# Kernel optimization log

Hardware: AMD Instinct MI355X
Metric: run time of the kernel (lower is better)

Reference implementation:

```python
import jax, jax.numpy as jnp
import numpy as np

N = 20000
E = 600000
D = 512
H = 8
HD = D // H
HID = 1024
FIN = D + 3 * H  # forces_mlp input dim = 536
SCALE = 1.0 / float(np.sqrt(HD))


def _ln(x, g, b, eps=1e-5):
    m = x.mean(-1, keepdims=True)
    v = x.var(-1, keepdims=True)
    return (x - m) / jnp.sqrt(v + eps) * g + b


def _resmlp(h, Wi, bi, Wh, bh, Wo, bo):
    # ResMLP with layers=3: in-proj, one residual hidden block, out-proj
    h = jax.nn.gelu(h @ Wi + bi)
    h = h + jax.nn.gelu(h @ Wh + bh)
    return h @ Wo + bo


def setup_inputs() -> dict:
    key = jax.random.key(0)
    ks = jax.random.split(key, 24)
    s = 0.02
    x = jax.random.normal(ks[0], (N, D), jnp.float32)
    edge_index = jax.random.randint(ks[1], (2, E), 0, N, dtype=jnp.int32)
    att_bias = jax.random.normal(ks[2], (E,), jnp.float32)
    pos = jax.random.normal(ks[3], (N, 3), jnp.float32)
    batch = jnp.zeros((N,), jnp.int32)
    return {
        "x": x, "edge_index": edge_index, "att_bias": att_bias, "pos": pos, "batch": batch,
        "g_att": jnp.ones((D,), jnp.float32), "b_att": jnp.zeros((D,), jnp.float32),
        "g_mlp": jnp.ones((D,), jnp.float32), "b_mlp": jnp.zeros((D,), jnp.float32),
        "Wq": jax.random.normal(ks[4], (D, D), jnp.float32) * s, "bq": jnp.zeros((D,), jnp.float32),
        "Wk": jax.random.normal(ks[5], (D, D), jnp.float32) * s, "bk": jnp.zeros((D,), jnp.float32),
        "We_in": jax.random.normal(ks[6], (D, HID), jnp.float32) * s, "be_in": jnp.zeros((HID,), jnp.float32),
        "We_h": jax.random.normal(ks[7], (HID, HID), jnp.float32) * s, "be_h": jnp.zeros((HID,), jnp.float32),
        "We_out": jax.random.normal(ks[8], (HID, 1), jnp.float32) * s, "be_out": jnp.zeros((1,), jnp.float32),
        "Wf_in": jax.random.normal(ks[9], (FIN, HID), jnp.float32) * s, "bf_in": jnp.zeros((HID,), jnp.float32),
        "Wf_h": jax.random.normal(ks[10], (HID, HID), jnp.float32) * s, "bf_h": jnp.zeros((HID,), jnp.float32),
        "Wf_out": jax.random.normal(ks[11], (HID, 3), jnp.float32) * s, "bf_out": jnp.zeros((3,), jnp.float32),
    }


def reference(x, edge_index, att_bias, pos, batch,
              g_att, b_att, g_mlp, b_mlp, Wq, bq, Wk, bk,
              We_in, be_in, We_h, be_h, We_out, be_out,
              Wf_in, bf_in, Wf_h, bf_h, Wf_out, bf_out):
    n = x.shape[0]
    row, col = edge_index[0], edge_index[1]

    z_att = _ln(x, g_att, b_att)
    q = (z_att @ Wq + bq).reshape(n, H, HD)  # [N,H,HD]
    k = (z_att @ Wk + bk).reshape(n, H, HD)

    # sparse scaled dot product restricted to edges, with additive per-edge bias
    logits = jnp.einsum('ehd,ehd->eh', q[row], k[col]) * SCALE + att_bias[:, None]  # [E,H]
    mx = jax.ops.segment_max(logits, row, num_segments=n)          # [N,H]
    mx = jnp.where(jnp.isfinite(mx), mx, 0.0)
    p = jnp.exp(logits - mx[row])
    denom = jax.ops.segment_sum(p, row, num_segments=n)            # [N,H]
    w = p / denom[row]                                             # [E,H]

    contrib = jnp.einsum('eh,ec->ehc', w, pos[col])                # [E,H,3]
    att = jax.ops.segment_sum(contrib, row, num_segments=n)        # [N,H,3]
    att = att - pos[:, None, :]                                    # att - value
    att = att.reshape(n, H * 3)                                    # permute(1,0,2).view(N,-1)

    z_mlp = _ln(x, g_mlp, b_mlp)
    energy = _resmlp(z_mlp, We_in, be_in, We_h, be_h, We_out, be_out)
    forces = _resmlp(jnp.concatenate([z_mlp, att], axis=-1), Wf_in, bf_in, Wf_h, bf_h, Wf_out, bf_out)
    return (energy, forces)
```

## Files before the change

### kernel.cpp

```cpp
#include <hip/hip_runtime.h>

#define NN 20000
#define EE 600000

typedef unsigned short u16;
typedef unsigned int u32;
typedef float f32x4 __attribute__((ext_vector_type(4)));
typedef u32 u32x4 __attribute__((ext_vector_type(4)));

__device__ __forceinline__ u16 f2bf(float f){
  u32 u = __float_as_uint(f);
  return (u16)((u + 0x7fffu + ((u>>16)&1u))>>16);
}
__device__ __forceinline__ float bf2f(u16 h){ return __uint_as_float(((u32)h)<<16); }

__device__ __forceinline__ float gelu_f(float x){
  float u = 0.7978845608028654f*(x + 0.044715f*x*x*x);
  float e = __expf(2.0f*u);
  return 0.5f*x*(2.0f - 2.0f/(e+1.0f));
}

__global__ __launch_bounds__(256) void ln2_kernel(
    const float* __restrict__ x,
    const float* __restrict__ ga, const float* __restrict__ ba,
    const float* __restrict__ gm, const float* __restrict__ bm,
    u16* __restrict__ za, u16* __restrict__ xf, int N)
{
  int row = (blockIdx.x<<2) + (threadIdx.x>>6);
  int lane = threadIdx.x & 63;
  if(row >= N) return;
  const float* xp = x + ((size_t)row<<9) + (lane<<3);
  f32x4 v0 = *(const f32x4*)xp;
  f32x4 v1 = *(const f32x4*)(xp+4);
  float vals[8] = {v0[0],v0[1],v0[2],v0[3],v1[0],v1[1],v1[2],v1[3]};
  float s=0.f, qs=0.f;
#pragma unroll
  for(int i=0;i<8;i++){ s += vals[i]; qs = fmaf(vals[i],vals[i],qs); }
#pragma unroll
  for(int o=1;o<64;o<<=1){ s += __shfl_xor(s,o); qs += __shfl_xor(qs,o); }
  float mean = s*(1.f/512.f);
  float var  = qs*(1.f/512.f) - mean*mean;
  float rstd = rsqrtf(var + 1e-5f);
  int c0 = lane<<3;
#pragma unroll
  for(int i=0;i<8;i++){
    float zn = (vals[i]-mean)*rstd;
    za[((size_t)row<<9)+c0+i]  = f2bf(fmaf(zn, ga[c0+i], ba[c0+i]));
    xf[(size_t)row*576+c0+i]   = f2bf(fmaf(zn, gm[c0+i], bm[c0+i]));
  }
}

__global__ __launch_bounds__(256) void wtt_kernel(
    const float* __restrict__ W, u16* __restrict__ WT, int K, int Nn, int Kpad)
{
  __shared__ u16 tile[64][65];
  const int k0 = blockIdx.x<<6, n0 = blockIdx.y<<6;
  const int tx = threadIdx.x & 63, ty = threadIdx.x >> 6;
#pragma unroll
  for(int i=0;i<16;i++){
    int r = (i<<2) + ty;
    int gk = k0 + r;
    float v = (gk < K) ? W[(size_t)gk*Nn + n0 + tx] : 0.f;
    tile[r][tx] = f2bf(v);
  }
  __syncthreads();
#pragma unroll
  for(int i=0;i<16;i++){
    int r = (i<<2) + ty;
    WT[(size_t)(n0 + r)*Kpad + k0 + tx] = tile[tx][r];
  }
}

__global__ __launch_bounds__(256) void gemm_bt(
    const u16* __restrict__ A, const u16* __restrict__ B,
    const float* __restrict__ bias, const u16* __restrict__ resid,
    u16* __restrict__ Cb, const float* __restrict__ wout,
    float* __restrict__ outp,
    int M, int N, int K, int lda, int ldr, int mode)
{
  __shared__ u16 As[128*64];
  __shared__ u16 Bs[128*64];
  const int gx = gridDim.x;
  const int b  = blockIdx.y*gx + blockIdx.x;
  const int xcd = b & 7, loc = b >> 3;
  const int tileM = ((loc/gx)*8 + xcd) << 7;
  const int tileN = (loc % gx) << 7;
  if(tileM >= M) return;
  const int tid  = threadIdx.x;
  const int wave = tid>>6, lane = tid&63;
  const int quad = lane>>4, l15 = lane&15;
  const int mhalf = (wave>>1)<<6, nhalf = (wave&1)<<6;
  f32x4 acc[4][4] = {};

  for(int k0=0; k0<K; k0+=64){
#pragma unroll
    for(int j=0;j<4;j++){
      const int c   = (((wave<<2)+j)<<6) + lane;
      const int row = c>>3;
      const int cc  = (c&7) ^ (row&7);
      int gr = tileM + row; gr = (gr < M) ? gr : (M-1);
      const u16* gp = A + (size_t)gr*lda + (size_t)(k0 + (cc<<3));
      __builtin_amdgcn_global_load_lds(
        (const __attribute__((address_space(1))) u32*)gp,
        (__attribute__((address_space(3))) u32*)(&As[((wave<<2)+j)<<9]),
        16, 0, 0);
    }
#pragma unroll
    for(int j=0;j<4;j++){
      const int c   = (((wave<<2)+j)<<6) + lane;
      const int row = c>>3;
      const int cc  = (c&7) ^ (row&7);
      const u16* gp = B + (size_t)(tileN + row)*K + (size_t)(k0 + (cc<<3));
      __builtin_amdgcn_global_load_lds(
        (const __attribute__((address_space(1))) u32*)gp,
        (__attribute__((address_space(3))) u32*)(&Bs[((wave<<2)+j)<<9]),
        16, 0, 0);
    }
    __syncthreads();
#pragma unroll
    for(int ks=0;ks<2;ks++){
      const int ccol = (ks<<2) + quad;
      u32x4 af[4], bfr[4];
#pragma unroll
      for(int mi=0;mi<4;mi++){
        const int row = mhalf + (mi<<4) + l15;
        af[mi] = *(const u32x4*)&As[((row<<3) + (ccol ^ (row&7)))<<3];
      }
#pragma unroll
      for(int ni=0;ni<4;ni++){
        const int row = nhalf + (ni<<4) + l15;
        bfr[ni] = *(const u32x4*)&Bs[((row<<3) + (ccol ^ (row&7)))<<3];
      }
#pragma unroll
      for(int mi=0;mi<4;mi++)
#pragma unroll
        for(int ni=0;ni<4;ni++)
          asm("v_mfma_f32_16x16x32_bf16 %0, %1, %2, %0"
              : "+v"(acc[mi][ni]) : "v"(af[mi]), "v"(bfr[ni]));
    }
    __syncthreads();
  }

  if(mode <= 1){
#pragma unroll
    for(int mi=0;mi<4;mi++){
#pragma unroll
      for(int reg=0;reg<4;reg++){
        const int gr = tileM + mhalf + (mi<<4) + (quad<<2) + reg;
        if(gr < M){
#pragma unroll
          for(int ni=0;ni<4;ni++){
            const int gc = tileN + nhalf + (ni<<4) + l15;
            float v = acc[mi][ni][reg] + bias[gc];
            if(mode == 1) v = gelu_f(v);
            Cb[(size_t)gr*N + gc] = f2bf(v);
          }
        }
      }
    }
  } else if(mode == 2){
    float wv[4], bv[4];
#pragma unroll
    for(int ni=0;ni<4;ni++){
      int gc = tileN + nhalf + (ni<<4) + l15;
      wv[ni] = wout[gc]; bv[ni] = bias[gc];
    }
#pragma unroll
    for(int mi=0;mi<4;mi++){
#pragma unroll
      for(int reg=0;reg<4;reg++){
        const int gr = tileM + mhalf + (mi<<4) + (quad<<2) + reg;
        if(gr < M){
          float vs = 0.f;
#pragma unroll
          for(int ni=0;ni<4;ni++){
            const int gc = tileN + nhalf + (ni<<4) + l15;
            float v = gelu_f(acc[mi][ni][reg] + bv[ni])
                    + bf2f(resid[(size_t)gr*ldr + gc]);
            vs = fmaf(v, wv[ni], vs);
          }
          vs += __shfl_xor(vs,1); vs += __shfl_xor(vs,2);
          vs += __shfl_xor(vs,4); vs += __shfl_xor(vs,8);
          if(l15 == 0) atomicAdd(&outp[gr], vs);
        }
      }
    }
  } else {
    float wv0[4], wv1[4], wv2[4], bv[4];
#pragma unroll
    for(int ni=0;ni<4;ni++){
      int gc = tileN + nhalf + (ni<<4) + l15;
      wv0[ni] = wout[gc*3+0]; wv1[ni] = wout[gc*3+1]; wv2[ni] = wout[gc*3+2];
      bv[ni] = bias[gc];
    }
#pragma unroll
    for(int mi=0;mi<4;mi++){
#pragma unroll
      for(int reg=0;reg<4;reg++){
        const int gr = tileM + mhalf + (mi<<4) + (quad<<2) + reg;
        if(gr < M){
          float s0=0.f, s1=0.f, s2=0.f;
#pragma unroll
          for(int ni=0;ni<4;ni++){
            const int gc = tileN + nhalf + (ni<<4) + l15;
            float v = gelu_f(acc[mi][ni][reg] + bv[ni])
                    + bf2f(resid[(size_t)gr*ldr + gc]);
            s0 = fmaf(v, wv0[ni], s0);
            s1 = fmaf(v, wv1[ni], s1);
            s2 = fmaf(v, wv2[ni], s2);
          }
          s0 += __shfl_xor(s0,1); s0 += __shfl_xor(s0,2); s0 += __shfl_xor(s0,4); s0 += __shfl_xor(s0,8);
          s1 += __shfl_xor(s1,1); s1 += __shfl_xor(s1,2); s1 += __shfl_xor(s1,4); s1 += __shfl_xor(s1,8);
          s2 += __shfl_xor(s2,1); s2 += __shfl_xor(s2,2); s2 += __shfl_xor(s2,4); s2 += __shfl_xor(s2,8);
          if(l15 == 0){
            atomicAdd(&outp[(size_t)gr*3+0], s0);
            atomicAdd(&outp[(size_t)gr*3+1], s1);
            atomicAdd(&outp[(size_t)gr*3+2], s2);
          }
        }
      }
    }
  }
}

__global__ __launch_bounds__(256) void out_init_kernel(
    float* __restrict__ out, const float* __restrict__ beO,
    const float* __restrict__ bfO)
{
  int idx = blockIdx.x*256 + threadIdx.x;
  if(idx < NN) out[idx] = beO[0];
  else if(idx < NN*4) out[idx] = bfO[(idx - NN) % 3];
}

__global__ __launch_bounds__(256) void hist_kernel(
    const int* __restrict__ ei, int* __restrict__ deg, int E)
{
  int e = blockIdx.x*256 + threadIdx.x;
  if(e < E) atomicAdd(&deg[ei[e]], 1);
}

__global__ __launch_bounds__(1024) void scan_kernel(
    const int* __restrict__ deg, int* __restrict__ rowptr,
    int* __restrict__ cursor, int N)
{
  __shared__ int wsum[16];
  __shared__ int carry_s;
  const int tid = threadIdx.x, lane = tid & 63, wid = tid >> 6;
  if(tid == 0) carry_s = 0;
  __syncthreads();
  for(int base = 0; base < N; base += 1024){
    int idx = base + tid;
    int v = (idx < N) ? deg[idx] : 0;
    int s = v;
#pragma unroll
    for(int o=1;o<64;o<<=1){ int t = __shfl_up(s,o); if(lane>=o) s += t; }
    if(lane==63) wsum[wid] = s;
    __syncthreads();
    if(wid==0 && lane<16){
      int ws = wsum[lane];
      int t = ws;
#pragma unroll
      for(int o=1;o<16;o<<=1){ int u = __shfl_up(t,o); if(lane>=o) t += u; }
      wsum[lane] = t - ws;
    }
    __syncthreads();
    int ex = s - v + wsum[wid] + carry_s;
    if(idx < N){ rowptr[idx] = ex; cursor[idx] = ex; }
    __syncthreads();
    if(tid == 1023) carry_s += wsum[15] + s;
  }
  __syncthreads();
  if(tid == 0) rowptr[N] = carry_s;
}

__global__ __launch_bounds__(256) void scatter_kernel(
    const int* __restrict__ ei, const float* __restrict__ ab,
    int* __restrict__ cursor, int* __restrict__ cols,
    float* __restrict__ abs_, int E)
{
  int e = blockIdx.x*256 + threadIdx.x;
  if(e >= E) return;
  int r = ei[e];
  int p = atomicAdd(&cursor[r], 1);
  cols[p] = ei[EE + e];
  abs_[p] = ab[e];
}

__global__ __launch_bounds__(256) void node_att_kernel(
    const u16* __restrict__ qk, const int* __restrict__ rowptr,
    const int* __restrict__ cols, const float* __restrict__ abs_,
    const float* __restrict__ pos, u16* __restrict__ xf, int N)
{
  const int node = (blockIdx.x<<2) + (threadIdx.x>>6);
  const int lane = threadIdx.x & 63;
  if(node >= N) return;
  const int h = lane>>3, sub = lane&7;
  const u32x4 qv = *(const u32x4*)(qk + ((size_t)node<<10) + (lane<<3));
  const float posn = (sub<3) ? pos[node*3 + sub] : 0.f;
  const int j1 = rowptr[node+1];
  float den = 0.f, nm = 0.f;

  int j = rowptr[node];
  for(; j+3 < j1; j += 4){
    int c[4]; float abv[4], pv[4]; u32x4 kv[4];
#pragma unroll
    for(int t=0;t<4;t++){ c[t] = cols[j+t]; abv[t] = abs_[j+t]; }
#pragma unroll
    for(int t=0;t<4;t++){
      kv[t] = *(const u32x4*)(qk + ((size_t)c[t]<<10) + 512 + (lane<<3));
      pv[t] = (sub<3) ? pos[c[t]*3+sub] : 0.f;
    }
#pragma unroll
    for(int t=0;t<4;t++){
      float s = 0.f;
#pragma unroll
      for(int i=0;i<4;i++){
        s = fmaf(__uint_as_float(qv[i]<<16),         __uint_as_float(kv[t][i]<<16), s);
        s = fmaf(__uint_as_float(qv[i]&0xffff0000u), __uint_as_float(kv[t][i]&0xffff0000u), s);
      }
      s += __shfl_xor(s,1); s += __shfl_xor(s,2); s += __shfl_xor(s,4);
      float p = __expf(fmaf(s, 0.125f, abv[t]));
      den += p;
      nm = fmaf(p, pv[t], nm);
    }
  }
  for(; j < j1; j++){
    int c0 = cols[j];
    u32x4 kv0 = *(const u32x4*)(qk + ((size_t)c0<<10) + 512 + (lane<<3));
    float pv0 = (sub<3) ? pos[c0*3+sub] : 0.f;
    float s0=0.f;
#pragma unroll
    for(int i=0;i<4;i++){
      s0 = fmaf(__uint_as_float(qv[i]<<16),        __uint_as_float(kv0[i]<<16), s0);
      s0 = fmaf(__uint_as_float(qv[i]&0xffff0000u),__uint_as_float(kv0[i]&0xffff0000u), s0);
    }
    s0 += __shfl_xor(s0,1); s0 += __shfl_xor(s0,2); s0 += __shfl_xor(s0,4);
    float p0 = __expf(fmaf(s0, 0.125f, abs_[j]));
    den += p0;
    nm = fmaf(p0, pv0, nm);
  }

  u16* xp = xf + (size_t)node*576;
  if(sub < 3){
    float a = (den > 0.f) ? nm/den : 0.f;
    xp[512 + h*3 + sub] = f2bf(a - posn);
  } else {
    xp[536 + h*5 + (sub-3)] = 0;
  }
}

extern "C" void kernel_launch(void* const* d_in, const int* in_sizes, int n_in,
                              void* d_out, int out_size, void* d_ws, size_t ws_size,
                              hipStream_t stream)
{
  (void)in_sizes; (void)n_in; (void)out_size; (void)ws_size;
  const float* x    = (const float*)d_in[0];
  const int*   ei   = (const int*)d_in[1];
  const float* ab   = (const float*)d_in[2];
  const float* pos  = (const float*)d_in[3];
  const float* g_att= (const float*)d_in[5];
  const float* b_att= (const float*)d_in[6];
  const float* g_mlp= (const float*)d_in[7];
  const float* b_mlp= (const float*)d_in[8];
  const float* Wq   = (const float*)d_in[9];  const float* bq  = (const float*)d_in[10];
  const float* Wk   = (const float*)d_in[11]; const float* bk  = (const float*)d_in[12];
  const float* WeI  = (const float*)d_in[13]; const float* beI = (const float*)d_in[14];
  const float* WeH  = (const float*)d_in[15]; const float* beH = (const float*)d_in[16];
  const float* WeO  = (const float*)d_in[17]; const float* beO = (const float*)d_in[18];
  const float* WfI  = (const float*)d_in[19]; const float* bfI = (const float*)d_in[20];
  const float* WfH  = (const float*)d_in[21]; const float* bfH = (const float*)d_in[22];
  const float* WfO  = (const float*)d_in[23]; const float* bfO = (const float*)d_in[24];

  char* w = (char*)d_ws;
  size_t off = 0;
  auto alloc = [&](size_t bytes) -> void* {
    void* p = w + off; off += (bytes + 255) & ~(size_t)255; return p;
  };
  u16* zatt  = (u16*)alloc((size_t)NN*512*2);
  u16* qk    = (u16*)alloc((size_t)NN*1024*2);
  u16* xf    = (u16*)alloc((size_t)NN*576*2);
  u16* h1cat = (u16*)alloc((size_t)NN*2048*2);
  u16* wqkT  = (u16*)alloc((size_t)1024*512*2);
  u16* wInT  = (u16*)alloc((size_t)2048*576*2);
  u16* weHT  = (u16*)alloc((size_t)1024*1024*2);
  u16* wfHT  = (u16*)alloc((size_t)1024*1024*2);
  float* bqk    = (float*)alloc((size_t)1024*4);
  float* bcat   = (float*)alloc((size_t)2048*4);
  int*   deg    = (int*)alloc((size_t)NN*4);
  int*   rowptr = (int*)alloc((size_t)(NN+1)*4);
  int*   cursor = (int*)alloc((size_t)NN*4);
  int*   cols   = (int*)alloc((size_t)EE*4);
  float* absrt  = (float*)alloc((size_t)EE*4);

  hipMemsetAsync(deg, 0, (size_t)NN*4, stream);
  hipMemcpyAsync(bqk,        bq,  512*4, hipMemcpyDeviceToDevice, stream);
  hipMemcpyAsync(bqk + 512,  bk,  512*4, hipMemcpyDeviceToDevice, stream);
  hipMemcpyAsync(bcat,       beI, 1024*4, hipMemcpyDeviceToDevice, stream);
  hipMemcpyAsync(bcat + 1024,bfI, 1024*4, hipMemcpyDeviceToDevice, stream);

  wtt_kernel<<<dim3(512/64, 512/64),256,0,stream>>>(Wq, wqkT,           512, 512, 512);
  wtt_kernel<<<dim3(512/64, 512/64),256,0,stream>>>(Wk, wqkT + 512*512, 512, 512, 512);
  wtt_kernel<<<dim3(576/64, 1024/64),256,0,stream>>>(WeI, wInT,              512, 1024, 576);
  wtt_kernel<<<dim3(576/64, 1024/64),256,0,stream>>>(WfI, wInT + 1024*576,   536, 1024, 576);
  wtt_kernel<<<dim3(1024/64,1024/64),256,0,stream>>>(WeH, weHT, 1024, 1024, 1024);
  wtt_kernel<<<dim3(1024/64,1024/64),256,0,stream>>>(WfH, wfHT, 1024, 1024, 1024);

  out_init_kernel<<<dim3((NN*4+255)/256),256,0,stream>>>((float*)d_out, beO, bfO);

  ln2_kernel<<<dim3((NN+3)/4),256,0,stream>>>(x, g_att,b_att, g_mlp,b_mlp, zatt, xf, NN);

  hist_kernel   <<<dim3((EE+255)/256),256,0,stream>>>(ei, deg, EE);
  scan_kernel   <<<1,1024,0,stream>>>(deg, rowptr, cursor, NN);
  scatter_kernel<<<dim3((EE+255)/256),256,0,stream>>>(ei, ab, cursor, cols, absrt, EE);

  const int MT = 160;

  gemm_bt<<<dim3(8, MT),256,0,stream>>>(zatt, wqkT, bqk, nullptr, qk,
                                        nullptr, nullptr, NN, 1024, 512, 512, 0, 0);

  node_att_kernel<<<dim3((NN+3)/4),256,0,stream>>>(qk, rowptr, cols, absrt, pos, xf, NN);

  gemm_bt<<<dim3(16, MT),256,0,stream>>>(xf, wInT, bcat, nullptr, h1cat,
                                         nullptr, nullptr, NN, 2048, 576, 576, 0, 1);

  gemm_bt<<<dim3(8, MT),256,0,stream>>>(h1cat, weHT, beH, h1cat, nullptr,
                                        WeO, (float*)d_out,
                                        NN, 1024, 1024, 2048, 2048, 2);
  gemm_bt<<<dim3(8, MT),256,0,stream>>>(h1cat+1024, wfHT, bfH, h1cat+1024, nullptr,
                                        WfO, (float*)d_out + NN,
                                        NN, 1024, 1024, 2048, 2048, 3);
}
```

Before: 639.0 us.

## Batch weight transposes and setup copies into fewer launches; unroll edge loop by 8

The six weight-transpose launches are merged into one 3D-grid kernel that reads per-matrix descriptors, with out-of-range blocks exiting early. The memset, four bias memcpys and the output-init kernel are folded into a single prep kernel. The per-node attention edge loop is unrolled from 4 to 8 edges so more gathers are in flight. Together these cut launch and API overhead and raise memory-level parallelism, at the cost of more registers in the attention kernel.

```diff
diff --git a/kernel.cpp b/kernel.cpp
--- a/kernel.cpp
+++ b/kernel.cpp
@@ -50,25 +50,45 @@
   }
 }
 
-__global__ __launch_bounds__(256) void wtt_kernel(
-    const float* __restrict__ W, u16* __restrict__ WT, int K, int Nn, int Kpad)
+struct WttDesc { const float* W; u16* WT; int K, Nn, Kpad; };
+struct WttPack { WttDesc d[6]; };
+
+__global__ __launch_bounds__(256) void wtt_all_kernel(WttPack p)
 {
   __shared__ u16 tile[64][65];
+  const WttDesc dd = p.d[blockIdx.z];
   const int k0 = blockIdx.x<<6, n0 = blockIdx.y<<6;
+  if(k0 >= dd.Kpad || n0 >= dd.Nn) return;
   const int tx = threadIdx.x & 63, ty = threadIdx.x >> 6;
 #pragma unroll
   for(int i=0;i<16;i++){
     int r = (i<<2) + ty;
     int gk = k0 + r;
-    float v = (gk < K) ? W[(size_t)gk*Nn + n0 + tx] : 0.f;
+    float v = (gk < dd.K) ? dd.W[(size_t)gk*dd.Nn + n0 + tx] : 0.f;
     tile[r][tx] = f2bf(v);
   }
   __syncthreads();
 #pragma unroll
   for(int i=0;i<16;i++){
     int r = (i<<2) + ty;
-    WT[(size_t)(n0 + r)*Kpad + k0 + tx] = tile[tx][r];
-  }
+    dd.WT[(size_t)(n0 + r)*dd.Kpad + k0 + tx] = tile[tx][r];
+  }
+}
+
+__global__ __launch_bounds__(256) void prep_kernel(
+    float* __restrict__ out, const float* __restrict__ beO, const float* __restrict__ bfO,
+    float* __restrict__ bqk, const float* __restrict__ bq, const float* __restrict__ bk,
+    float* __restrict__ bcat, const float* __restrict__ beI, const float* __restrict__ bfI,
+    int* __restrict__ deg)
+{
+  int idx = blockIdx.x*256 + threadIdx.x;
+  if(idx < NN) out[idx] = beO[0];
+  else if(idx < NN*4) out[idx] = bfO[(idx - NN) % 3];
+  if(idx < 512) bqk[idx] = bq[idx];
+  else if(idx < 1024) bqk[idx] = bk[idx-512];
+  if(idx < 1024) bcat[idx] = beI[idx];
+  else if(idx < 2048) bcat[idx] = bfI[idx-1024];
+  if(idx < NN) deg[idx] = 0;
 }
 
 __global__ __launch_bounds__(256) void gemm_bt(
@@ -223,15 +243,6 @@
   }
 }
 
-__global__ __launch_bounds__(256) void out_init_kernel(
-    float* __restrict__ out, const float* __restrict__ beO,
-    const float* __restrict__ bfO)
-{
-  int idx = blockIdx.x*256 + threadIdx.x;
-  if(idx < NN) out[idx] = beO[0];
-  else if(idx < NN*4) out[idx] = bfO[(idx - NN) % 3];
-}
-
 __global__ __launch_bounds__(256) void hist_kernel(
     const int* __restrict__ ei, int* __restrict__ deg, int E)
 {
@@ -301,17 +312,17 @@
   float den = 0.f, nm = 0.f;
 
   int j = rowptr[node];
-  for(; j+3 < j1; j += 4){
-    int c[4]; float abv[4], pv[4]; u32x4 kv[4];
-#pragma unroll
-    for(int t=0;t<4;t++){ c[t] = cols[j+t]; abv[t] = abs_[j+t]; }
-#pragma unroll
-    for(int t=0;t<4;t++){
+  for(; j+7 < j1; j += 8){
+    int c[8]; float abv[8], pv[8]; u32x4 kv[8];
+#pragma unroll
+    for(int t=0;t<8;t++){ c[t] = cols[j+t]; abv[t] = abs_[j+t]; }
+#pragma unroll
+    for(int t=0;t<8;t++){
       kv[t] = *(const u32x4*)(qk + ((size_t)c[t]<<10) + 512 + (lane<<3));
       pv[t] = (sub<3) ? pos[c[t]*3+sub] : 0.f;
     }
 #pragma unroll
-    for(int t=0;t<4;t++){
+    for(int t=0;t<8;t++){
       float s = 0.f;
 #pragma unroll
       for(int i=0;i<4;i++){
@@ -392,20 +403,17 @@
   int*   cols   = (int*)alloc((size_t)EE*4);
   float* absrt  = (float*)alloc((size_t)EE*4);
 
-  hipMemsetAsync(deg, 0, (size_t)NN*4, stream);
-  hipMemcpyAsync(bqk,        bq,  512*4, hipMemcpyDeviceToDevice, stream);
-  hipMemcpyAsync(bqk + 512,  bk,  512*4, hipMemcpyDeviceToDevice, stream);
-  hipMemcpyAsync(bcat,       beI, 1024*4, hipMemcpyDeviceToDevice, stream);
-  hipMemcpyAsync(bcat + 1024,bfI, 1024*4, hipMemcpyDeviceToDevice, stream);
-
-  wtt_kernel<<<dim3(512/64, 512/64),256,0,stream>>>(Wq, wqkT,           512, 512, 512);
-  wtt_kernel<<<dim3(512/64, 512/64),256,0,stream>>>(Wk, wqkT + 512*512, 512, 512, 512);
-  wtt_kernel<<<dim3(576/64, 1024/64),256,0,stream>>>(WeI, wInT,              512, 1024, 576);
-  wtt_kernel<<<dim3(576/64, 1024/64),256,0,stream>>>(WfI, wInT + 1024*576,   536, 1024, 576);
-  wtt_kernel<<<dim3(1024/64,1024/64),256,0,stream>>>(WeH, weHT, 1024, 1024, 1024);
-  wtt_kernel<<<dim3(1024/64,1024/64),256,0,stream>>>(WfH, wfHT, 1024, 1024, 1024);
-
-  out_init_kernel<<<dim3((NN*4+255)/256),256,0,stream>>>((float*)d_out, beO, bfO);
+  WttPack pk;
+  pk.d[0] = { Wq,  wqkT,            512,  512,  512 };
+  pk.d[1] = { Wk,  wqkT + 512*512,  512,  512,  512 };
+  pk.d[2] = { WeI, wInT,            512,  1024, 576 };
+  pk.d[3] = { WfI, wInT + 1024*576, 536,  1024, 576 };
+  pk.d[4] = { WeH, weHT,            1024, 1024, 1024 };
+  pk.d[5] = { WfH, wfHT,            1024, 1024, 1024 };
+  wtt_all_kernel<<<dim3(16, 16, 6),256,0,stream>>>(pk);
+
+  prep_kernel<<<dim3((NN*4+255)/256),256,0,stream>>>(
+      (float*)d_out, beO, bfO, bqk, bq, bk, bcat, beI, bfI, deg);
 
   ln2_kernel<<<dim3((NN+3)/4),256,0,stream>>>(x, g_att,b_att, g_mlp,b_mlp, zatt, xf, NN);
 
```

Measured after the change: 604.3 us. -5.4%, faster.
